# Optimization experiments

Hardware: AMD Instinct MI355X
Metric: run time of the kernel (lower is better)

## Reference

```python
import jax, jax.numpy as jnp
import numpy as np

D_MODEL = 1024
N_HEADS = 16
N_GROUPS = 4
D_K = D_MODEL // N_HEADS
HEADS_PER_GROUP = N_HEADS // N_GROUPS


def rope(x):
    # x: [b, s, d]; rotate using half-split concat (NOT interleaved), matching source
    s, d = x.shape[1], x.shape[2]
    theta = 1.0 / (10000.0 ** (jnp.arange(d // 2, dtype=jnp.float32) / (d // 2)))
    ang = jnp.arange(s, dtype=jnp.float32)[:, None] * theta[None, :]  # [s, d/2]
    cos, sin = jnp.cos(ang), jnp.sin(ang)
    xe, xo = x[..., 0::2], x[..., 1::2]
    return jnp.concatenate([xe * cos - xo * sin, xe * sin + xo * cos], axis=-1)


def setup_inputs() -> dict:
    key = jax.random.key(0)
    k1, k2, k3, k4, k5 = jax.random.split(key, 5)
    b, s = 1, 2048
    scale = 0.02
    X = jax.random.normal(k1, (b, s, D_MODEL), dtype=jnp.float32)
    W_q = jax.random.normal(k2, (D_MODEL, D_MODEL), dtype=jnp.float32) * scale
    W_k = jax.random.normal(k3, (N_GROUPS * D_K, D_MODEL), dtype=jnp.float32) * scale
    W_v = jax.random.normal(k4, (N_GROUPS * D_K, D_MODEL), dtype=jnp.float32) * scale
    W_o = jax.random.normal(k5, (D_MODEL, D_MODEL), dtype=jnp.float32) * scale
    return {"X": X, "W_q": W_q, "W_k": W_k, "W_v": W_v, "W_o": W_o}


def reference(X, W_q, W_k, W_v, W_o):
    b, s, _ = X.shape
    Xr = rope(X)
    Q = (Xr @ W_q.T).reshape(b, s, N_HEADS, D_K).transpose(0, 2, 1, 3)
    K = (Xr @ W_k.T).reshape(b, s, N_GROUPS, D_K).transpose(0, 2, 1, 3)
    V = (Xr @ W_v.T).reshape(b, s, N_GROUPS, D_K).transpose(0, 2, 1, 3)
    Q = Q.reshape(b, N_GROUPS, HEADS_PER_GROUP, s, D_K)
    scores = jnp.einsum('bghsd,bgtd->bghst', Q, K) / jnp.sqrt(jnp.float32(D_K))
    mask = jnp.triu(jnp.ones((s, s), dtype=scores.dtype), k=1) * (-1e9)
    attn = jax.nn.softmax(scores + mask, axis=-1)
    out = jnp.einsum('bghst,bgtd->bghsd', attn, V)  # [b,g,h,s,dk]
    out = out.reshape(b, N_HEADS, s, D_K).transpose(0, 2, 1, 3).reshape(b, s, D_MODEL)
    return out @ W_o.T
```

## Files before the change

kernel.cpp:

```cpp
#include <hip/hip_runtime.h>
#include <hip/hip_bf16.h>

#define S_LEN   2048
#define D_MODEL 1024
#define N_HEADS 16
#define N_GROUPS 4
#define D_K     64
#define KV_DIM  (N_GROUPS * D_K)

typedef __hip_bfloat16 bf16;
typedef unsigned short u16;
typedef __attribute__((ext_vector_type(8))) short bfrag;
typedef __attribute__((ext_vector_type(4))) float ffrag;
typedef __attribute__((ext_vector_type(4))) unsigned int u32x4;

__device__ __forceinline__ float b2f(u16 u) {
    return __uint_as_float(((unsigned)u) << 16);
}
__device__ __forceinline__ u16 f2bu(float f) {
    bf16 h = __float2bfloat16(f);
    return __builtin_bit_cast(u16, h);
}
__device__ __forceinline__ unsigned cvt_pk_bf16(float lo, float hi) {
    unsigned r;
    asm("v_cvt_pk_bf16_f32 %0, %1, %2" : "=v"(r) : "v"(lo), "v"(hi));
    return r;
}
__device__ __forceinline__ float max3f(float a, float b, float c) {
    float d;
    asm("v_max3_f32 %0, %1, %2, %3" : "=v"(d) : "v"(a), "v"(b), "v"(c));
    return d;
}
__device__ __forceinline__ float ex2(float x) {
#if __has_builtin(__builtin_amdgcn_exp2f)
    return __builtin_amdgcn_exp2f(x);
#else
    return __expf(x * 0.69314718f);
#endif
}

typedef __attribute__((address_space(3))) u16 lds_u16;
typedef __attribute__((address_space(1))) const u16 glb_u16;
__device__ __forceinline__ void gld_lds16(const u16* g, u16* l) {
    __builtin_amdgcn_global_load_lds((glb_u16*)g, (lds_u16*)l, 16, 0, 0);
}

__device__ __forceinline__ int probe_f32(const u16* p) {
    int lane = threadIdx.x & 63;
    int e0 = (p[lane] >> 7) & 0xFF;
    int e1 = (p[lane + 64] >> 7) & 0xFF;
    int c = ((e0 < 100 || e0 > 140) ? 1 : 0) + ((e1 < 100 || e1 > 140) ? 1 : 0);
    unsigned long long b1 = __ballot(c >= 1);
    unsigned long long b2 = __ballot(c >= 2);
    return ((__popcll(b1) + __popcll(b2)) > 16) ? 1 : 0;
}

__global__ void probe5_kernel(const u16* __restrict__ p0, const u16* __restrict__ p1,
                              const u16* __restrict__ p2, const u16* __restrict__ p3,
                              const u16* __restrict__ p4, int* __restrict__ mode) {
    if (blockIdx.x != 0) return;
    const u16* ps[5] = {p0, p1, p2, p3, p4};
    int lane = threadIdx.x & 63;
    for (int t = 0; t < 5; t++) {
        int e0 = (ps[t][lane] >> 7) & 0xFF;
        int e1 = (ps[t][lane + 64] >> 7) & 0xFF;
        int c = ((e0 < 100 || e0 > 140) ? 1 : 0) + ((e1 < 100 || e1 > 140) ? 1 : 0);
        unsigned long long b1 = __ballot(c >= 1);
        unsigned long long b2 = __ballot(c >= 2);
        if (lane == 0) mode[t] = ((__popcll(b1) + __popcll(b2)) > 16) ? 1 : 0;
    }
}

__global__ __launch_bounds__(512)
void prep_kernel(const void* __restrict__ Xin, u16* __restrict__ Xr,
                 const void* __restrict__ Wq, const void* __restrict__ Wk,
                 const void* __restrict__ Wv, const void* __restrict__ Wo,
                 u16* __restrict__ WB, u16* __restrict__ WoB) {
    int b = blockIdx.x;
    if (b < S_LEN) {
        int md = probe_f32((const u16*)Xin);
        int i = b;
        int j = threadIdx.x;
        float freq = ex2(-(float)j * 0.025952563241307518f);
        float ang  = (float)i * freq;
        float sv, cv;
        sincosf(ang, &sv, &cv);
        int base = i * D_MODEL;
        float xe, xo;
        if (md) {
            float2 xv = *(const float2*)&((const float*)Xin)[base + 2 * j];
            xe = xv.x; xo = xv.y;
        } else {
            ushort2 xv = *(const ushort2*)&((const u16*)Xin)[base + 2 * j];
            xe = b2f(xv.x); xo = b2f(xv.y);
        }
        Xr[base + j]       = f2bu(xe * cv - xo * sv);
        Xr[base + 512 + j] = f2bu(xe * sv + xo * cv);
    } else {
        int bid = b - S_LEN;
        const void* src; u16* dst; int goff;
        if (bid < 256)      { src = Wq; dst = WB;               goff = bid; }
        else if (bid < 320) { src = Wk; dst = WB + 1024 * 1024; goff = bid - 256; }
        else if (bid < 384) { src = Wv; dst = WB + 1280 * 1024; goff = bid - 320; }
        else                { src = Wo; dst = WoB;              goff = bid - 384; }
        int md = probe_f32((const u16*)src);
        size_t g = (size_t)goff * 512 + threadIdx.x;
        if (md) {
            const float* f = (const float*)src + g * 8;
            float4 v0 = *(const float4*)f;
            float4 v1 = *(const float4*)(f + 4);
            u16 t[8] = {f2bu(v0.x), f2bu(v0.y), f2bu(v0.z), f2bu(v0.w),
                        f2bu(v1.x), f2bu(v1.y), f2bu(v1.z), f2bu(v1.w)};
            *(uint4*)(dst + g * 8) = *(const uint4*)t;
        } else {
            *(uint4*)(dst + g * 8) = *(const uint4*)((const u16*)src + g * 8);
        }
    }
}

__global__ __launch_bounds__(512)
void rope_kernel(const void* __restrict__ Xin, u16* __restrict__ Xr) {
    int md = probe_f32((const u16*)Xin);
    int i = blockIdx.x;
    int j = threadIdx.x;
    float freq = ex2(-(float)j * 0.025952563241307518f);
    float ang  = (float)i * freq;
    float sv, cv;
    sincosf(ang, &sv, &cv);
    int base = i * D_MODEL;
    float xe, xo;
    if (md) {
        float2 xv = *(const float2*)&((const float*)Xin)[base + 2 * j];
        xe = xv.x; xo = xv.y;
    } else {
        ushort2 xv = *(const ushort2*)&((const u16*)Xin)[base + 2 * j];
        xe = b2f(xv.x); xo = b2f(xv.y);
    }
    Xr[base + j]       = f2bu(xe * cv - xo * sv);
    Xr[base + 512 + j] = f2bu(xe * sv + xo * cv);
}

template<int MODE>
__global__ __launch_bounds__(256)
void gemm_fast(const u16* __restrict__ A, const u16* __restrict__ WBm,
               u16* __restrict__ Qm, u16* __restrict__ Km, u16* __restrict__ Vm,
               float* __restrict__ Cf) {
    __shared__ u16 As[2][8192];
    __shared__ u16 Bs[2][4096];
    const int tid = threadIdx.x;
    const int w = tid >> 6, lane = tid & 63, quad = lane >> 4, lcol = lane & 15;

    const int flat = blockIdx.y * gridDim.x + blockIdx.x;
    const int cpx  = (gridDim.x * gridDim.y) >> 3;
    const int ns   = (flat & 7) * cpx + (flat >> 3);
    const int m0 = (ns / gridDim.x) * 128;
    const int n0 = (ns % gridDim.x) * 64;

    const int arl   = lane >> 3;
    const int colsw = ((lane & 7) ^ arl) * 8;

    const u16* ap[4]; const u16* bp[2];
    #pragma unroll
    for (int c = 0; c < 4; c++)
        ap[c] = A + (size_t)(m0 + (c * 4 + w) * 8 + arl) * 1024 + colsw;
    #pragma unroll
    for (int c = 0; c < 2; c++)
        bp[c] = WBm + (size_t)(n0 + (c * 4 + w) * 8 + arl) * 1024 + colsw;

    const int abase = (w * 32 + lcol) * 64;
    const int koff0 = (quad * 8) ^ ((lcol & 7) * 8);
    const int koff1 = koff0 ^ 32;

    ffrag acc[2][4];
    #pragma unroll
    for (int rf = 0; rf < 2; rf++)
        #pragma unroll
        for (int ct = 0; ct < 4; ct++) acc[rf][ct] = (ffrag)0.0f;

    #pragma unroll
    for (int c = 0; c < 4; c++) gld_lds16(ap[c], &As[0][(c * 4 + w) * 512]);
    #pragma unroll
    for (int c = 0; c < 2; c++) gld_lds16(bp[c], &Bs[0][(c * 4 + w) * 512]);
    __syncthreads();

    int cur = 0;
    for (int k0 = 0; k0 < D_MODEL; k0 += 64) {
        if (k0 + 64 < D_MODEL) {
            const int nb = cur ^ 1;
            #pragma unroll
            for (int c = 0; c < 4; c++)
                gld_lds16(ap[c] + k0 + 64, &As[nb][(c * 4 + w) * 512]);
            #pragma unroll
            for (int c = 0; c < 2; c++)
                gld_lds16(bp[c] + k0 + 64, &Bs[nb][(c * 4 + w) * 512]);
        }

        const u16* Ab = &As[cur][0];
        const u16* Bb = &Bs[cur][0];
        const bfrag a00 = *(const bfrag*)&Ab[abase + koff0];
        const bfrag a10 = *(const bfrag*)&Ab[abase + 1024 + koff0];
        const bfrag a01 = *(const bfrag*)&Ab[abase + koff1];
        const bfrag a11 = *(const bfrag*)&Ab[abase + 1024 + koff1];
        #pragma unroll
        for (int ct = 0; ct < 4; ct++) {
            const int bb = (ct * 16 + lcol) * 64;
            const bfrag b0 = *(const bfrag*)&Bb[bb + koff0];
            acc[0][ct] = __builtin_amdgcn_mfma_f32_16x16x32_bf16(a00, b0, acc[0][ct], 0, 0, 0);
            acc[1][ct] = __builtin_amdgcn_mfma_f32_16x16x32_bf16(a10, b0, acc[1][ct], 0, 0, 0);
            const bfrag b1 = *(const bfrag*)&Bb[bb + koff1];
            acc[0][ct] = __builtin_amdgcn_mfma_f32_16x16x32_bf16(a01, b1, acc[0][ct], 0, 0, 0);
            acc[1][ct] = __builtin_amdgcn_mfma_f32_16x16x32_bf16(a11, b1, acc[1][ct], 0, 0, 0);
        }
        __syncthreads();
        cur ^= 1;
    }

    if (MODE == 0) {
        if (n0 < 1280) {
            u16* Cp; int ldc, nc;
            if (n0 < 1024) { Cp = Qm; ldc = 1024; nc = n0; }
            else           { Cp = Km; ldc = 256;  nc = n0 - 1024; }
            #pragma unroll
            for (int rf = 0; rf < 2; rf++)
                #pragma unroll
                for (int ct = 0; ct < 4; ct++)
                    #pragma unroll
                    for (int r = 0; r < 4; r++) {
                        int row = m0 + w * 32 + rf * 16 + quad * 4 + r;
                        Cp[(size_t)row * ldc + nc + ct * 16 + lcol] = f2bu(acc[rf][ct][r]);
                    }
        } else {
            const int nc = n0 - 1280;
            #pragma unroll
            for (int rf = 0; rf < 2; rf++)
                #pragma unroll
                for (int ct = 0; ct < 4; ct++)
                    #pragma unroll
                    for (int r = 0; r < 4; r++) {
                        int row = m0 + w * 32 + rf * 16 + quad * 4 + r;
                        int col = nc + ct * 16 + lcol;
                        Vm[(size_t)col * S_LEN + row] = f2bu(acc[rf][ct][r]);
                    }
        }
    } else {
        #pragma unroll
        for (int rf = 0; rf < 2; rf++)
            #pragma unroll
            for (int ct = 0; ct < 4; ct++)
                #pragma unroll
                for (int r = 0; r < 4; r++) {
                    int row = m0 + w * 32 + rf * 16 + quad * 4 + r;
                    Cf[(size_t)row * D_MODEL + n0 + ct * 16 + lcol] = acc[rf][ct][r];
                }
    }
}

__device__ __forceinline__ void stageB(u16* dst, const void* Bv, size_t off, int md) {
    if (md) {
        const float* Bf = (const float*)Bv;
        float4 b0 = *(const float4*)&Bf[off];
        float4 b1 = *(const float4*)&Bf[off + 4];
        u16 t[8] = {f2bu(b0.x), f2bu(b0.y), f2bu(b0.z), f2bu(b0.w),
                    f2bu(b1.x), f2bu(b1.y), f2bu(b1.z), f2bu(b1.w)};
        *(uint4*)dst = *(const uint4*)t;
    } else {
        *(uint4*)dst = *(const uint4*)&((const u16*)Bv)[off];
    }
}

__global__ __launch_bounds__(256)
void qkv_mfma(const u16* __restrict__ Xr, const void* __restrict__ Wq,
              const void* __restrict__ Wk, const void* __restrict__ Wv,
              u16* __restrict__ Qm, u16* __restrict__ Km, u16* __restrict__ Vm,
              const int* __restrict__ mode) {
    __shared__ u16 As[128][36];
    __shared__ u16 Bs[64][36];
    const int tid = threadIdx.x;
    const int w = tid >> 6, lane = tid & 63, quad = lane >> 4, lcol = lane & 15;
    const int m0 = blockIdx.y * 128;
    const int n0 = blockIdx.x * 64;

    const void* Bv; int nb, md;
    if (n0 < 1024)       { Bv = Wq; nb = n0;        md = mode[1]; }
    else if (n0 < 1280)  { Bv = Wk; nb = n0 - 1024; md = mode[2]; }
    else                 { Bv = Wv; nb = n0 - 1280; md = mode[3]; }

    ffrag acc[2][4];
    #pragma unroll
    for (int rf = 0; rf < 2; rf++)
        #pragma unroll
        for (int ct = 0; ct < 4; ct++) acc[rf][ct] = (ffrag)0.0f;

    const int arow = tid >> 2, akc = tid & 3;
    for (int k0 = 0; k0 < D_MODEL; k0 += 32) {
        *(uint4*)&As[arow][akc * 8] =
            *(const uint4*)&Xr[(size_t)(m0 + arow) * D_MODEL + k0 + akc * 8];
        *(uint4*)&As[arow + 64][akc * 8] =
            *(const uint4*)&Xr[(size_t)(m0 + arow + 64) * D_MODEL + k0 + akc * 8];
        stageB(&Bs[arow][akc * 8], Bv, (size_t)(nb + arow) * D_MODEL + k0 + akc * 8, md);
        __syncthreads();
        const bfrag a0 = *(const bfrag*)&As[w * 32 + lcol][quad * 8];
        const bfrag a1 = *(const bfrag*)&As[w * 32 + 16 + lcol][quad * 8];
        #pragma unroll
        for (int ct = 0; ct < 4; ct++) {
            const bfrag b = *(const bfrag*)&Bs[ct * 16 + lcol][quad * 8];
            acc[0][ct] = __builtin_amdgcn_mfma_f32_16x16x32_bf16(a0, b, acc[0][ct], 0, 0, 0);
            acc[1][ct] = __builtin_amdgcn_mfma_f32_16x16x32_bf16(a1, b, acc[1][ct], 0, 0, 0);
        }
        __syncthreads();
    }

    if (n0 < 1280) {
        u16* Cp; int ldc, nc;
        if (n0 < 1024) { Cp = Qm; ldc = 1024; nc = n0; }
        else           { Cp = Km; ldc = 256;  nc = n0 - 1024; }
        #pragma unroll
        for (int rf = 0; rf < 2; rf++)
            #pragma unroll
            for (int ct = 0; ct < 4; ct++)
                #pragma unroll
                for (int r = 0; r < 4; r++) {
                    int row = m0 + w * 32 + rf * 16 + quad * 4 + r;
                    Cp[(size_t)row * ldc + nc + ct * 16 + lcol] = f2bu(acc[rf][ct][r]);
                }
    } else {
        const int nc = n0 - 1280;
        #pragma unroll
        for (int rf = 0; rf < 2; rf++)
            #pragma unroll
            for (int ct = 0; ct < 4; ct++)
                #pragma unroll
                for (int r = 0; r < 4; r++) {
                    int row = m0 + w * 32 + rf * 16 + quad * 4 + r;
                    int col = nc + ct * 16 + lcol;
                    Vm[(size_t)col * S_LEN + row] = f2bu(acc[rf][ct][r]);
                }
    }
}

__global__ __launch_bounds__(256)
void oproj_mfma(const u16* __restrict__ A, const void* __restrict__ B,
                float* __restrict__ C, const int* __restrict__ mode) {
    __shared__ u16 As[128][36];
    __shared__ u16 Bs[64][36];
    const int tid = threadIdx.x;
    const int w = tid >> 6, lane = tid & 63, quad = lane >> 4, lcol = lane & 15;
    const int m0 = blockIdx.y * 128;
    const int n0 = blockIdx.x * 64;
    const int md = mode[4];

    ffrag acc[2][4];
    #pragma unroll
    for (int rf = 0; rf < 2; rf++)
        #pragma unroll
        for (int ct = 0; ct < 4; ct++) acc[rf][ct] = (ffrag)0.0f;

    const int arow = tid >> 2, akc = tid & 3;
    for (int k0 = 0; k0 < D_MODEL; k0 += 32) {
        *(uint4*)&As[arow][akc * 8] =
            *(const uint4*)&A[(size_t)(m0 + arow) * D_MODEL + k0 + akc * 8];
        *(uint4*)&As[arow + 64][akc * 8] =
            *(const uint4*)&A[(size_t)(m0 + arow + 64) * D_MODEL + k0 + akc * 8];
        stageB(&Bs[arow][akc * 8], B, (size_t)(n0 + arow) * D_MODEL + k0 + akc * 8, md);
        __syncthreads();
        const bfrag a0 = *(const bfrag*)&As[w * 32 + lcol][quad * 8];
        const bfrag a1 = *(const bfrag*)&As[w * 32 + 16 + lcol][quad * 8];
        #pragma unroll
        for (int ct = 0; ct < 4; ct++) {
            const bfrag b = *(const bfrag*)&Bs[ct * 16 + lcol][quad * 8];
            acc[0][ct] = __builtin_amdgcn_mfma_f32_16x16x32_bf16(a0, b, acc[0][ct], 0, 0, 0);
            acc[1][ct] = __builtin_amdgcn_mfma_f32_16x16x32_bf16(a1, b, acc[1][ct], 0, 0, 0);
        }
        __syncthreads();
    }

    #pragma unroll
    for (int rf = 0; rf < 2; rf++)
        #pragma unroll
        for (int ct = 0; ct < 4; ct++)
            #pragma unroll
            for (int r = 0; r < 4; r++) {
                int row = m0 + w * 32 + rf * 16 + quad * 4 + r;
                C[(size_t)row * D_MODEL + n0 + ct * 16 + lcol] = acc[rf][ct][r];
            }
}

template<int CS, int SF>
__global__ __launch_bounds__(256)
void attn_part(const u16* __restrict__ Q, const u16* __restrict__ K,
               const u16* __restrict__ Vt, float* __restrict__ OpF,
               u16* __restrict__ OpH, float2* __restrict__ ml2) {
    const int bid = blockIdx.x;
    const int cidx = bid >> 4;
    const int h = bid & 15;
    const int g = h >> 2;

    int i, c;
    if (CS == 3) {
        if (cidx < 8)       { i = cidx;                  c = 0; }
        else if (cidx < 24) { i = 8 + ((cidx - 8) >> 1); c = (cidx - 8) & 1; }
        else if (cidx < 48) { int q = (cidx - 24) / 3;   i = 16 + q; c = (cidx - 24) - 3 * q; }
        else                { i = 24 + ((cidx - 48) >> 2); c = (cidx - 48) & 3; }
    } else {
        if (cidx < 16) { i = cidx; c = 0; }
        else           { i = 16 + ((cidx - 16) >> 1); c = (cidx - 16) & 1; }
    }
    const int i0 = i * 64;
    const int tile0 = c << CS;
    const int tlast = min(i, ((c + 1) << CS) - 1);
    const int nt = tlast - tile0 + 1;

    const int tid  = threadIdx.x;
    const int w    = tid >> 6;
    const int lane = tid & 63;
    const int quad = lane >> 4;
    const int lcol = lane & 15;

    __shared__ u16 Ks[2][64][72];
    __shared__ u16 Vts[2][64][72];

    const int qi = i0 + w * 16 + lcol;
    const bfrag qb0 = *(const bfrag*)&Q[(size_t)qi * D_MODEL + h * 64 + quad * 8];
    const bfrag qb1 = *(const bfrag*)&Q[(size_t)qi * D_MODEL + h * 64 + 32 + quad * 8];

    ffrag oacc[4];
    #pragma unroll
    for (int ct = 0; ct < 4; ct++) oacc[ct] = (ffrag)0.0f;
    float m_run = -1e30f, l_run = 0.0f;

    const int key0 = tid & 63, dc0 = tid >> 6;
    const int vd0 = tid >> 3, vch = tid & 7;
    const int vpos0 = 32 * (vch >> 2) + 16 * (vch & 1) + 4 * ((vch >> 1) & 1);
    const u16* vbase0 = &Vt[(size_t)(g * 64 + vd0) * S_LEN];
    const u16* vbase1 = &Vt[(size_t)(g * 64 + vd0 + 32) * S_LEN];

    int jp = tile0 * 64;
    uint4 kpre0 = *(const uint4*)&K[(size_t)(jp + key0) * KV_DIM + g * 64 + dc0 * 8];
    uint4 kpre1 = *(const uint4*)&K[(size_t)(jp + key0) * KV_DIM + g * 64 + (dc0 + 4) * 8];
    uint4 vpre0 = *(const uint4*)&vbase0[jp + vch * 8];
    uint4 vpre1 = *(const uint4*)&vbase1[jp + vch * 8];

    {
        *(uint4*)&Ks[0][key0][dc0 * 8]       = kpre0;
        *(uint4*)&Ks[0][key0][(dc0 + 4) * 8] = kpre1;
        *(uint2*)&Vts[0][vd0][vpos0]          = make_uint2(vpre0.x, vpre0.y);
        *(uint2*)&Vts[0][vd0][vpos0 + 8]      = make_uint2(vpre0.z, vpre0.w);
        *(uint2*)&Vts[0][vd0 + 32][vpos0]     = make_uint2(vpre1.x, vpre1.y);
        *(uint2*)&Vts[0][vd0 + 32][vpos0 + 8] = make_uint2(vpre1.z, vpre1.w);
    }

    const float CF = 0.18033688f;
    int cur = 0;

    for (int tt = 0; tt < nt; tt++) {
        const int j0 = (tile0 + tt) * 64;

        if (tt + 1 < nt) {
            const int j0n = (tile0 + tt + 1) * 64;
            kpre0 = *(const uint4*)&K[(size_t)(j0n + key0) * KV_DIM + g * 64 + dc0 * 8];
            kpre1 = *(const uint4*)&K[(size_t)(j0n + key0) * KV_DIM + g * 64 + (dc0 + 4) * 8];
            vpre0 = *(const uint4*)&vbase0[j0n + vch * 8];
            vpre1 = *(const uint4*)&vbase1[j0n + vch * 8];
        }
        __syncthreads();

        ffrag sacc[4];
        #pragma unroll
        for (int ct = 0; ct < 4; ct++) sacc[ct] = (ffrag)0.0f;
        __builtin_amdgcn_s_setprio(1);
        #pragma unroll
        for (int ct = 0; ct < 4; ct++) {
            const bfrag kb0 = *(const bfrag*)&Ks[cur][ct * 16 + lcol][quad * 8];
            sacc[ct] = __builtin_amdgcn_mfma_f32_16x16x32_bf16(kb0, qb0, sacc[ct], 0, 0, 0);
            const bfrag kb1 = *(const bfrag*)&Ks[cur][ct * 16 + lcol][32 + quad * 8];
            sacc[ct] = __builtin_amdgcn_mfma_f32_16x16x32_bf16(kb1, qb1, sacc[ct], 0, 0, 0);
        }
        __builtin_amdgcn_s_setprio(0);

        float sv[4][4];
        if (tile0 + tt == i) {
            #pragma unroll
            for (int ct = 0; ct < 4; ct++)
                #pragma unroll
                for (int r = 0; r < 4; r++) {
                    int kj = j0 + ct * 16 + quad * 4 + r;
                    sv[ct][r] = (kj <= qi) ? sacc[ct][r] : -1e30f;
                }
        } else {
            #pragma unroll
            for (int ct = 0; ct < 4; ct++)
                #pragma unroll
                for (int r = 0; r < 4; r++) sv[ct][r] = sacc[ct][r];
        }

        float t0 = max3f(sv[0][0], sv[0][1], sv[0][2]);
        float t1 = max3f(sv[0][3], sv[1][0], sv[1][1]);
        float t2 = max3f(sv[1][2], sv[1][3], sv[2][0]);
        float t3 = max3f(sv[2][1], sv[2][2], sv[2][3]);
        float t4 = max3f(sv[3][0], sv[3][1], sv[3][2]);
        float mx = fmaxf(max3f(t0, t1, t2), max3f(t3, t4, sv[3][3]));
        mx = fmaxf(mx, __shfl_xor(mx, 16, 64));
        mx = fmaxf(mx, __shfl_xor(mx, 32, 64));

        if (!__all(mx <= m_run + 44.0f)) {
            float mnew = fmaxf(m_run, mx);
            float al = ex2((m_run - mnew) * CF);
            m_run = mnew;
            l_run *= al;
            #pragma unroll
            for (int r = 0; r < 4; r++) {
                float ar = __shfl(al, quad * 4 + r, 64);
                #pragma unroll
                for (int ct = 0; ct < 4; ct++) oacc[ct][r] *= ar;
            }
        }

        const float mc = m_run * CF;
        float rs = 0.0f;
        #pragma unroll
        for (int ct = 0; ct < 4; ct++)
            #pragma unroll
            for (int r = 0; r < 4; r++) {
                float p = ex2(sv[ct][r] * CF - mc);
                sv[ct][r] = p;
                rs += p;
            }
        rs += __shfl_xor(rs, 16, 64);
        rs += __shfl_xor(rs, 32, 64);
        l_run += rs;

        u32x4 pw0, pw1;
        pw0[0] = cvt_pk_bf16(sv[0][0], sv[0][1]);
        pw0[1] = cvt_pk_bf16(sv[0][2], sv[0][3]);
        pw0[2] = cvt_pk_bf16(sv[1][0], sv[1][1]);
        pw0[3] = cvt_pk_bf16(sv[1][2], sv[1][3]);
        pw1[0] = cvt_pk_bf16(sv[2][0], sv[2][1]);
        pw1[1] = cvt_pk_bf16(sv[2][2], sv[2][3]);
        pw1[2] = cvt_pk_bf16(sv[3][0], sv[3][1]);
        pw1[3] = cvt_pk_bf16(sv[3][2], sv[3][3]);
        const bfrag pa0 = __builtin_bit_cast(bfrag, pw0);
        const bfrag pa1 = __builtin_bit_cast(bfrag, pw1);

        __builtin_amdgcn_s_setprio(1);
        #pragma unroll
        for (int ct = 0; ct < 4; ct++) {
            const bfrag vb0 = *(const bfrag*)&Vts[cur][ct * 16 + lcol][quad * 8];
            oacc[ct] = __builtin_amdgcn_mfma_f32_16x16x32_bf16(pa0, vb0, oacc[ct], 0, 0, 0);
            const bfrag vb1 = *(const bfrag*)&Vts[cur][ct * 16 + lcol][32 + quad * 8];
            oacc[ct] = __builtin_amdgcn_mfma_f32_16x16x32_bf16(pa1, vb1, oacc[ct], 0, 0, 0);
        }
        __builtin_amdgcn_s_setprio(0);

        if (tt + 1 < nt) {
            const int nb = cur ^ 1;
            *(uint4*)&Ks[nb][key0][dc0 * 8]       = kpre0;
            *(uint4*)&Ks[nb][key0][(dc0 + 4) * 8] = kpre1;
            *(uint2*)&Vts[nb][vd0][vpos0]          = make_uint2(vpre0.x, vpre0.y);
            *(uint2*)&Vts[nb][vd0][vpos0 + 8]      = make_uint2(vpre0.z, vpre0.w);
            *(uint2*)&Vts[nb][vd0 + 32][vpos0]     = make_uint2(vpre1.x, vpre1.y);
            *(uint2*)&Vts[nb][vd0 + 32][vpos0 + 8] = make_uint2(vpre1.z, vpre1.w);
        }
        cur ^= 1;
    }

    #pragma unroll
    for (int ct = 0; ct < 4; ct++)
        #pragma unroll
        for (int r = 0; r < 4; r++) {
            int row = w * 16 + quad * 4 + r;
            size_t off = (size_t)bid * 4096 + row * 64 + ct * 16 + lcol;
            if (SF) OpF[off] = oacc[ct][r];
            else    OpH[off] = f2bu(oacc[ct][r]);
        }
    if (quad == 0)
        ml2[(size_t)bid * 64 + w * 16 + lcol] = make_float2(m_run * 0.125f, l_run);
}

template<int CS, int SF>
__global__ __launch_bounds__(256)
void attn_combine(const float* __restrict__ OpF, const u16* __restrict__ OpH,
                  const float2* __restrict__ ml2, u16* __restrict__ Om) {
    const int row = blockIdx.x;
    const int i = row >> 6;
    const int r = row & 63;
    const int t = threadIdx.x;
    const int h = t >> 4;
    const int d = (t & 15) * 4;
    const int nc = (i >> CS) + 1;
    int pfx;
    if (CS == 3)
        pfx = (i < 8) ? i : (i < 16) ? 8 + 2 * (i - 8)
            : (i < 24) ? 24 + 3 * (i - 16) : 48 + 4 * (i - 24);
    else
        pfx = (i < 16) ? i : 16 + 2 * (i - 16);

    float M = -1e30f;
    for (int c = 0; c < nc; c++) {
        float2 m = ml2[(size_t)((pfx + c) * 16 + h) * 64 + r];
        M = fmaxf(M, m.x);
    }
    float L = 0.0f;
    float acc[4] = {0.0f, 0.0f, 0.0f, 0.0f};
    for (int c = 0; c < nc; c++) {
        float2 m = ml2[(size_t)((pfx + c) * 16 + h) * 64 + r];
        float wgt = __expf(m.x - M);
        L += m.y * wgt;
        size_t off = (size_t)((pfx + c) * 16 + h) * 4096 + r * 64 + d;
        if (SF) {
            float4 v = *(const float4*)&OpF[off];
            acc[0] += v.x * wgt; acc[1] += v.y * wgt;
            acc[2] += v.z * wgt; acc[3] += v.w * wgt;
        } else {
            ushort4 v = *(const ushort4*)&OpH[off];
            acc[0] += b2f(v.x) * wgt; acc[1] += b2f(v.y) * wgt;
            acc[2] += b2f(v.z) * wgt; acc[3] += b2f(v.w) * wgt;
        }
    }
    float inv = 1.0f / L;
    #pragma unroll
    for (int k = 0; k < 4; k++)
        Om[(size_t)row * D_MODEL + h * 64 + d + k] = f2bu(acc[k] * inv);
}

extern "C" void kernel_launch(void* const* d_in, const int* in_sizes, int n_in,
                              void* d_out, int out_size, void* d_ws, size_t ws_size,
                              hipStream_t stream) {
    const void* X  = d_in[0];
    const void* Wq = d_in[1];
    const void* Wk = d_in[2];
    const void* Wv = d_in[3];
    const void* Wo = d_in[4];
    float* out = (float*)d_out;

    u16* XrB = (u16*)d_out;

    int* mode = (int*)d_ws;
    u16* Qm = (u16*)((char*)d_ws + 64);
    u16* Km = Qm + (size_t)S_LEN * D_MODEL;
    u16* Vm = Km + (size_t)S_LEN * KV_DIM;
    u16* Om = Vm + (size_t)S_LEN * KV_DIM;

    const size_t needA    = 10485824ULL + 20971520ULL + 655360ULL;
    const size_t needFull = needA + 3145728ULL + 2097152ULL;

    if (ws_size >= needFull) {
        float*  OpF = (float*)((char*)d_ws + 10485824);
        float2* ml2 = (float2*)((char*)d_ws + 10485824 + 20971520);
        u16*    WB  = (u16*)((char*)d_ws + needA);
        u16*    WoB = WB + (size_t)1536 * 1024;

        prep_kernel<<<S_LEN + 640, 512, 0, stream>>>(X, XrB, Wq, Wk, Wv, Wo, WB, WoB);
        gemm_fast<0><<<dim3(24, 16), 256, 0, stream>>>(XrB, WB, Qm, Km, Vm, nullptr);
        attn_part<3, 1><<<80 * 16, 256, 0, stream>>>(Qm, Km, Vm, OpF, nullptr, ml2);
        attn_combine<3, 1><<<S_LEN, 256, 0, stream>>>(OpF, nullptr, ml2, Om);
        gemm_fast<1><<<dim3(16, 16), 256, 0, stream>>>(Om, WoB, nullptr, nullptr, nullptr, out);
    } else {
        rope_kernel<<<S_LEN, 512, 0, stream>>>(X, XrB);
        probe5_kernel<<<1, 64, 0, stream>>>(
            (const u16*)X, (const u16*)Wq, (const u16*)Wk, (const u16*)Wv,
            (const u16*)Wo, mode);
        qkv_mfma<<<dim3((D_MODEL + 2 * KV_DIM) / 64, S_LEN / 128), 256, 0, stream>>>(
            XrB, Wq, Wk, Wv, Qm, Km, Vm, mode);
        if (ws_size >= needA) {
            float*  OpF = (float*)((char*)d_ws + 10485824);
            float2* ml2 = (float2*)((char*)d_ws + 10485824 + 20971520);
            attn_part<3, 1><<<80 * 16, 256, 0, stream>>>(Qm, Km, Vm, OpF, nullptr, ml2);
            attn_combine<3, 1><<<S_LEN, 256, 0, stream>>>(OpF, nullptr, ml2, Om);
        } else {
            u16*    OpH = (u16*)d_out;
            float2* ml2 = (float2*)((char*)d_out + (size_t)768 * 4096 * 2);
            attn_part<4, 0><<<48 * 16, 256, 0, stream>>>(Qm, Km, Vm, nullptr, OpH, ml2);
            attn_combine<4, 0><<<S_LEN, 256, 0, stream>>>(nullptr, OpH, ml2, Om);
        }
        oproj_mfma<<<dim3(D_MODEL / 64, S_LEN / 128), 256, 0, stream>>>(Om, Wo, out, mode);
    }
}
```

Baseline: 141.2 us.

## Schedule full attention chunks longest-first and defer softmax rescale past PV MFMA

Reorders the split-KV attention block mapping so full 8-tile chunks are launched before the partial diagonal chunks, ordered from largest work down. The combine kernel gets a matching position function. This is meant to reduce tail imbalance across CUs. It also starts the running max at zero and moves the online-softmax rescale after the P·V MFMAs, so the rescale branch no longer sits on the critical path before the exponentials. The trade-off is that probabilities are briefly computed against a stale max and may reach large magnitudes before they are rescaled.

```diff
diff --git a/kernel.cpp b/kernel.cpp
--- a/kernel.cpp
+++ b/kernel.cpp
@@ -43,6 +43,13 @@
 typedef __attribute__((address_space(1))) const u16 glb_u16;
 __device__ __forceinline__ void gld_lds16(const u16* g, u16* l) {
     __builtin_amdgcn_global_load_lds((glb_u16*)g, (lds_u16*)l, 16, 0, 0);
+}
+
+__device__ __forceinline__ int pos3(int i, int c) {
+    int d = i - 8 * c;
+    if (d >= 7)
+        return (c == 0) ? i - 7 : (c == 1) ? 10 + i : (c == 2) ? 19 + i : 51;
+    return 52 + (6 - d) * 4 + c;
 }
 
 __device__ __forceinline__ int probe_f32(const u16* p) {
@@ -397,10 +404,11 @@
 
     int i, c;
     if (CS == 3) {
-        if (cidx < 8)       { i = cidx;                  c = 0; }
-        else if (cidx < 24) { i = 8 + ((cidx - 8) >> 1); c = (cidx - 8) & 1; }
-        else if (cidx < 48) { int q = (cidx - 24) / 3;   i = 16 + q; c = (cidx - 24) - 3 * q; }
-        else                { i = 24 + ((cidx - 48) >> 2); c = (cidx - 48) & 3; }
+        if (cidx < 25)       { c = 0; i = cidx + 7; }
+        else if (cidx < 42)  { c = 1; i = cidx - 10; }
+        else if (cidx < 51)  { c = 2; i = cidx - 19; }
+        else if (cidx == 51) { c = 3; i = 31; }
+        else { int t = cidx - 52; int dd = 6 - (t >> 2); c = t & 3; i = 8 * c + dd; }
     } else {
         if (cidx < 16) { i = cidx; c = 0; }
         else           { i = 16 + ((cidx - 16) >> 1); c = (cidx - 16) & 1; }
@@ -426,7 +434,7 @@
     ffrag oacc[4];
     #pragma unroll
     for (int ct = 0; ct < 4; ct++) oacc[ct] = (ffrag)0.0f;
-    float m_run = -1e30f, l_run = 0.0f;
+    float m_run = 0.0f, l_run = 0.0f;
 
     const int key0 = tid & 63, dc0 = tid >> 6;
     const int vd0 = tid >> 3, vch = tid & 7;
@@ -501,19 +509,6 @@
         float mx = fmaxf(max3f(t0, t1, t2), max3f(t3, t4, sv[3][3]));
         mx = fmaxf(mx, __shfl_xor(mx, 16, 64));
         mx = fmaxf(mx, __shfl_xor(mx, 32, 64));
-
-        if (!__all(mx <= m_run + 44.0f)) {
-            float mnew = fmaxf(m_run, mx);
-            float al = ex2((m_run - mnew) * CF);
-            m_run = mnew;
-            l_run *= al;
-            #pragma unroll
-            for (int r = 0; r < 4; r++) {
-                float ar = __shfl(al, quad * 4 + r, 64);
-                #pragma unroll
-                for (int ct = 0; ct < 4; ct++) oacc[ct][r] *= ar;
-            }
-        }
 
         const float mc = m_run * CF;
         float rs = 0.0f;
@@ -551,6 +546,19 @@
         }
         __builtin_amdgcn_s_setprio(0);
 
+        if (!__all(mx <= m_run + 44.0f)) {
+            float mnew = fmaxf(m_run, mx);
+            float al = ex2((m_run - mnew) * CF);
+            l_run *= al;
+            #pragma unroll
+            for (int r = 0; r < 4; r++) {
+                float ar = __shfl(al, quad * 4 + r, 64);
+                #pragma unroll
+                for (int ct = 0; ct < 4; ct++) oacc[ct][r] *= ar;
+            }
+            m_run = mnew;
+        }
+
         if (tt + 1 < nt) {
             const int nb = cur ^ 1;
             *(uint4*)&Ks[nb][key0][dc0 * 8]       = kpre0;
@@ -587,25 +595,21 @@
     const int h = t >> 4;
     const int d = (t & 15) * 4;
     const int nc = (i >> CS) + 1;
-    int pfx;
-    if (CS == 3)
-        pfx = (i < 8) ? i : (i < 16) ? 8 + 2 * (i - 8)
-            : (i < 24) ? 24 + 3 * (i - 16) : 48 + 4 * (i - 24);
-    else
-        pfx = (i < 16) ? i : 16 + 2 * (i - 16);
 
     float M = -1e30f;
     for (int c = 0; c < nc; c++) {
-        float2 m = ml2[(size_t)((pfx + c) * 16 + h) * 64 + r];
+        int pos = (CS == 3) ? pos3(i, c) : ((i < 16) ? i : 16 + 2 * (i - 16)) + c;
+        float2 m = ml2[(size_t)(pos * 16 + h) * 64 + r];
         M = fmaxf(M, m.x);
     }
     float L = 0.0f;
     float acc[4] = {0.0f, 0.0f, 0.0f, 0.0f};
     for (int c = 0; c < nc; c++) {
-        float2 m = ml2[(size_t)((pfx + c) * 16 + h) * 64 + r];
+        int pos = (CS == 3) ? pos3(i, c) : ((i < 16) ? i : 16 + 2 * (i - 16)) + c;
+        float2 m = ml2[(size_t)(pos * 16 + h) * 64 + r];
         float wgt = __expf(m.x - M);
         L += m.y * wgt;
-        size_t off = (size_t)((pfx + c) * 16 + h) * 4096 + r * 64 + d;
+        size_t off = (size_t)(pos * 16 + h) * 4096 + r * 64 + d;
         if (SF) {
             float4 v = *(const float4*)&OpF[off];
             acc[0] += v.x * wgt; acc[1] += v.y * wgt;
```

Measured after the change: 138.7 us. No clear change (-1.8%).

## Process 128 query rows per attention block to reuse K/V tiles

Applied to the files above, without the earlier changes.

Each attention work item now covers two 64-row query tiles (A and B) that share every K/V tile loaded into LDS, which halves the number of K/V loads and blocks. The causal chunk scheduling and the combine kernel's indexing are remapped for 128-row items, with a reordered work list so that longer chunks are issued first. Softmax rescaling is deferred until after the PV MFMA, starting from a running max of zero. Launch bounds request 4 waves per SIMD. Register pressure roughly doubles and there are half as many blocks, which may reduce occupancy and parallelism.

```diff
diff --git a/kernel.cpp b/kernel.cpp
--- a/kernel.cpp
+++ b/kernel.cpp
@@ -43,6 +43,13 @@
 typedef __attribute__((address_space(1))) const u16 glb_u16;
 __device__ __forceinline__ void gld_lds16(const u16* g, u16* l) {
     __builtin_amdgcn_global_load_lds((glb_u16*)g, (lds_u16*)l, 16, 0, 0);
+}
+
+__device__ __forceinline__ int posCS3(int i, int c) {
+    if (i >= 4 * c + 3)
+        return (c == 0) ? i - 3 : (c == 1) ? i + 6 : (c == 2) ? i + 11 : 27;
+    int dd = i - 4 * c + 1;
+    return 28 + (3 - dd) * 4 + c;
 }
 
 __device__ __forceinline__ int probe_f32(const u16* p) {
@@ -386,7 +393,7 @@
 }
 
 template<int CS, int SF>
-__global__ __launch_bounds__(256)
+__global__ __launch_bounds__(256, 4)
 void attn_part(const u16* __restrict__ Q, const u16* __restrict__ K,
                const u16* __restrict__ Vt, float* __restrict__ OpF,
                u16* __restrict__ OpH, float2* __restrict__ ml2) {
@@ -397,17 +404,18 @@
 
     int i, c;
     if (CS == 3) {
-        if (cidx < 8)       { i = cidx;                  c = 0; }
-        else if (cidx < 24) { i = 8 + ((cidx - 8) >> 1); c = (cidx - 8) & 1; }
-        else if (cidx < 48) { int q = (cidx - 24) / 3;   i = 16 + q; c = (cidx - 24) - 3 * q; }
-        else                { i = 24 + ((cidx - 48) >> 2); c = (cidx - 48) & 3; }
+        if (cidx < 13)       { c = 0; i = cidx + 3; }
+        else if (cidx < 22)  { c = 1; i = cidx - 6; }
+        else if (cidx < 27)  { c = 2; i = cidx - 11; }
+        else if (cidx == 27) { c = 3; i = 15; }
+        else { int t = cidx - 28; int dd = 3 - (t >> 2); c = t & 3; i = 4 * c + dd - 1; }
     } else {
-        if (cidx < 16) { i = cidx; c = 0; }
-        else           { i = 16 + ((cidx - 16) >> 1); c = (cidx - 16) & 1; }
-    }
-    const int i0 = i * 64;
+        if (cidx < 8) { i = cidx; c = 0; }
+        else          { i = 8 + ((cidx - 8) >> 1); c = (cidx - 8) & 1; }
+    }
+    const int i0 = i * 128;
     const int tile0 = c << CS;
-    const int tlast = min(i, ((c + 1) << CS) - 1);
+    const int tlast = min(2 * i + 1, ((c + 1) << CS) - 1);
     const int nt = tlast - tile0 + 1;
 
     const int tid  = threadIdx.x;
@@ -419,14 +427,18 @@
     __shared__ u16 Ks[2][64][72];
     __shared__ u16 Vts[2][64][72];
 
-    const int qi = i0 + w * 16 + lcol;
-    const bfrag qb0 = *(const bfrag*)&Q[(size_t)qi * D_MODEL + h * 64 + quad * 8];
-    const bfrag qb1 = *(const bfrag*)&Q[(size_t)qi * D_MODEL + h * 64 + 32 + quad * 8];
-
-    ffrag oacc[4];
-    #pragma unroll
-    for (int ct = 0; ct < 4; ct++) oacc[ct] = (ffrag)0.0f;
-    float m_run = -1e30f, l_run = 0.0f;
+    const int qiA = i0 + w * 16 + lcol;
+    const int qiB = qiA + 64;
+    const bfrag qbA0 = *(const bfrag*)&Q[(size_t)qiA * D_MODEL + h * 64 + quad * 8];
+    const bfrag qbA1 = *(const bfrag*)&Q[(size_t)qiA * D_MODEL + h * 64 + 32 + quad * 8];
+    const bfrag qbB0 = *(const bfrag*)&Q[(size_t)qiB * D_MODEL + h * 64 + quad * 8];
+    const bfrag qbB1 = *(const bfrag*)&Q[(size_t)qiB * D_MODEL + h * 64 + 32 + quad * 8];
+
+    ffrag oaccA[4], oaccB[4];
+    #pragma unroll
+    for (int ct = 0; ct < 4; ct++) { oaccA[ct] = (ffrag)0.0f; oaccB[ct] = (ffrag)0.0f; }
+    float m_runA = 0.0f, l_runA = 0.0f;
+    float m_runB = 0.0f, l_runB = 0.0f;
 
     const int key0 = tid & 63, dc0 = tid >> 6;
     const int vd0 = tid >> 3, vch = tid & 7;
@@ -453,10 +465,11 @@
     int cur = 0;
 
     for (int tt = 0; tt < nt; tt++) {
-        const int j0 = (tile0 + tt) * 64;
+        const int tj = tile0 + tt;
+        const int j0 = tj * 64;
 
         if (tt + 1 < nt) {
-            const int j0n = (tile0 + tt + 1) * 64;
+            const int j0n = (tj + 1) * 64;
             kpre0 = *(const uint4*)&K[(size_t)(j0n + key0) * KV_DIM + g * 64 + dc0 * 8];
             kpre1 = *(const uint4*)&K[(size_t)(j0n + key0) * KV_DIM + g * 64 + (dc0 + 4) * 8];
             vpre0 = *(const uint4*)&vbase0[j0n + vch * 8];
@@ -464,92 +477,157 @@
         }
         __syncthreads();
 
-        ffrag sacc[4];
-        #pragma unroll
-        for (int ct = 0; ct < 4; ct++) sacc[ct] = (ffrag)0.0f;
+        ffrag saccA[4], saccB[4];
+        #pragma unroll
+        for (int ct = 0; ct < 4; ct++) { saccA[ct] = (ffrag)0.0f; saccB[ct] = (ffrag)0.0f; }
         __builtin_amdgcn_s_setprio(1);
         #pragma unroll
         for (int ct = 0; ct < 4; ct++) {
             const bfrag kb0 = *(const bfrag*)&Ks[cur][ct * 16 + lcol][quad * 8];
-            sacc[ct] = __builtin_amdgcn_mfma_f32_16x16x32_bf16(kb0, qb0, sacc[ct], 0, 0, 0);
+            saccA[ct] = __builtin_amdgcn_mfma_f32_16x16x32_bf16(kb0, qbA0, saccA[ct], 0, 0, 0);
+            saccB[ct] = __builtin_amdgcn_mfma_f32_16x16x32_bf16(kb0, qbB0, saccB[ct], 0, 0, 0);
             const bfrag kb1 = *(const bfrag*)&Ks[cur][ct * 16 + lcol][32 + quad * 8];
-            sacc[ct] = __builtin_amdgcn_mfma_f32_16x16x32_bf16(kb1, qb1, sacc[ct], 0, 0, 0);
+            saccA[ct] = __builtin_amdgcn_mfma_f32_16x16x32_bf16(kb1, qbA1, saccA[ct], 0, 0, 0);
+            saccB[ct] = __builtin_amdgcn_mfma_f32_16x16x32_bf16(kb1, qbB1, saccB[ct], 0, 0, 0);
         }
         __builtin_amdgcn_s_setprio(0);
 
-        float sv[4][4];
-        if (tile0 + tt == i) {
+        float svA[4][4];
+        if (tj >= 2 * i) {
             #pragma unroll
             for (int ct = 0; ct < 4; ct++)
                 #pragma unroll
                 for (int r = 0; r < 4; r++) {
                     int kj = j0 + ct * 16 + quad * 4 + r;
-                    sv[ct][r] = (kj <= qi) ? sacc[ct][r] : -1e30f;
+                    svA[ct][r] = (kj <= qiA) ? saccA[ct][r] : -1e30f;
                 }
         } else {
             #pragma unroll
             for (int ct = 0; ct < 4; ct++)
                 #pragma unroll
-                for (int r = 0; r < 4; r++) sv[ct][r] = sacc[ct][r];
-        }
-
-        float t0 = max3f(sv[0][0], sv[0][1], sv[0][2]);
-        float t1 = max3f(sv[0][3], sv[1][0], sv[1][1]);
-        float t2 = max3f(sv[1][2], sv[1][3], sv[2][0]);
-        float t3 = max3f(sv[2][1], sv[2][2], sv[2][3]);
-        float t4 = max3f(sv[3][0], sv[3][1], sv[3][2]);
-        float mx = fmaxf(max3f(t0, t1, t2), max3f(t3, t4, sv[3][3]));
-        mx = fmaxf(mx, __shfl_xor(mx, 16, 64));
-        mx = fmaxf(mx, __shfl_xor(mx, 32, 64));
-
-        if (!__all(mx <= m_run + 44.0f)) {
-            float mnew = fmaxf(m_run, mx);
-            float al = ex2((m_run - mnew) * CF);
-            m_run = mnew;
-            l_run *= al;
+                for (int r = 0; r < 4; r++) svA[ct][r] = saccA[ct][r];
+        }
+        float tA0 = max3f(svA[0][0], svA[0][1], svA[0][2]);
+        float tA1 = max3f(svA[0][3], svA[1][0], svA[1][1]);
+        float tA2 = max3f(svA[1][2], svA[1][3], svA[2][0]);
+        float tA3 = max3f(svA[2][1], svA[2][2], svA[2][3]);
+        float tA4 = max3f(svA[3][0], svA[3][1], svA[3][2]);
+        float mxA = fmaxf(max3f(tA0, tA1, tA2), max3f(tA3, tA4, svA[3][3]));
+        mxA = fmaxf(mxA, __shfl_xor(mxA, 16, 64));
+        mxA = fmaxf(mxA, __shfl_xor(mxA, 32, 64));
+
+        const float mcA = m_runA * CF;
+        float rsA = 0.0f;
+        #pragma unroll
+        for (int ct = 0; ct < 4; ct++)
+            #pragma unroll
+            for (int r = 0; r < 4; r++) {
+                float p = ex2(svA[ct][r] * CF - mcA);
+                svA[ct][r] = p;
+                rsA += p;
+            }
+        rsA += __shfl_xor(rsA, 16, 64);
+        rsA += __shfl_xor(rsA, 32, 64);
+        l_runA += rsA;
+
+        u32x4 pwA0, pwA1;
+        pwA0[0] = cvt_pk_bf16(svA[0][0], svA[0][1]);
+        pwA0[1] = cvt_pk_bf16(svA[0][2], svA[0][3]);
+        pwA0[2] = cvt_pk_bf16(svA[1][0], svA[1][1]);
+        pwA0[3] = cvt_pk_bf16(svA[1][2], svA[1][3]);
+        pwA1[0] = cvt_pk_bf16(svA[2][0], svA[2][1]);
+        pwA1[1] = cvt_pk_bf16(svA[2][2], svA[2][3]);
+        pwA1[2] = cvt_pk_bf16(svA[3][0], svA[3][1]);
+        pwA1[3] = cvt_pk_bf16(svA[3][2], svA[3][3]);
+        const bfrag paA0 = __builtin_bit_cast(bfrag, pwA0);
+        const bfrag paA1 = __builtin_bit_cast(bfrag, pwA1);
+
+        float svB[4][4];
+        if (tj == 2 * i + 1) {
+            #pragma unroll
+            for (int ct = 0; ct < 4; ct++)
+                #pragma unroll
+                for (int r = 0; r < 4; r++) {
+                    int kj = j0 + ct * 16 + quad * 4 + r;
+                    svB[ct][r] = (kj <= qiB) ? saccB[ct][r] : -1e30f;
+                }
+        } else {
+            #pragma unroll
+            for (int ct = 0; ct < 4; ct++)
+                #pragma unroll
+                for (int r = 0; r < 4; r++) svB[ct][r] = saccB[ct][r];
+        }
+        float tB0 = max3f(svB[0][0], svB[0][1], svB[0][2]);
+        float tB1 = max3f(svB[0][3], svB[1][0], svB[1][1]);
+        float tB2 = max3f(svB[1][2], svB[1][3], svB[2][0]);
+        float tB3 = max3f(svB[2][1], svB[2][2], svB[2][3]);
+        float tB4 = max3f(svB[3][0], svB[3][1], svB[3][2]);
+        float mxB = fmaxf(max3f(tB0, tB1, tB2), max3f(tB3, tB4, svB[3][3]));
+        mxB = fmaxf(mxB, __shfl_xor(mxB, 16, 64));
+        mxB = fmaxf(mxB, __shfl_xor(mxB, 32, 64));
+
+        const float mcB = m_runB * CF;
+        float rsB = 0.0f;
+        #pragma unroll
+        for (int ct = 0; ct < 4; ct++)
+            #pragma unroll
+            for (int r = 0; r < 4; r++) {
+                float p = ex2(svB[ct][r] * CF - mcB);
+                svB[ct][r] = p;
+                rsB += p;
+            }
+        rsB += __shfl_xor(rsB, 16, 64);
+        rsB += __shfl_xor(rsB, 32, 64);
+        l_runB += rsB;
+
+        u32x4 pwB0, pwB1;
+        pwB0[0] = cvt_pk_bf16(svB[0][0], svB[0][1]);
+        pwB0[1] = cvt_pk_bf16(svB[0][2], svB[0][3]);
+        pwB0[2] = cvt_pk_bf16(svB[1][0], svB[1][1]);
+        pwB0[3] = cvt_pk_bf16(svB[1][2], svB[1][3]);
+        pwB1[0] = cvt_pk_bf16(svB[2][0], svB[2][1]);
+        pwB1[1] = cvt_pk_bf16(svB[2][2], svB[2][3]);
+        pwB1[2] = cvt_pk_bf16(svB[3][0], svB[3][1]);
+        pwB1[3] = cvt_pk_bf16(svB[3][2], svB[3][3]);
+        const bfrag paB0 = __builtin_bit_cast(bfrag, pwB0);
+        const bfrag paB1 = __builtin_bit_cast(bfrag, pwB1);
+
+        __builtin_amdgcn_s_setprio(1);
+        #pragma unroll
+        for (int ct = 0; ct < 4; ct++) {
+            const bfrag vb0 = *(const bfrag*)&Vts[cur][ct * 16 + lcol][quad * 8];
+            oaccA[ct] = __builtin_amdgcn_mfma_f32_16x16x32_bf16(paA0, vb0, oaccA[ct], 0, 0, 0);
+            oaccB[ct] = __builtin_amdgcn_mfma_f32_16x16x32_bf16(paB0, vb0, oaccB[ct], 0, 0, 0);
+            const bfrag vb1 = *(const bfrag*)&Vts[cur][ct * 16 + lcol][32 + quad * 8];
+            oaccA[ct] = __builtin_amdgcn_mfma_f32_16x16x32_bf16(paA1, vb1, oaccA[ct], 0, 0, 0);
+            oaccB[ct] = __builtin_amdgcn_mfma_f32_16x16x32_bf16(paB1, vb1, oaccB[ct], 0, 0, 0);
+        }
+        __builtin_amdgcn_s_setprio(0);
+
+        if (!__all(mxA <= m_runA + 44.0f)) {
+            float mnew = fmaxf(m_runA, mxA);
+            float al = ex2((m_runA - mnew) * CF);
+            l_runA *= al;
             #pragma unroll
             for (int r = 0; r < 4; r++) {
                 float ar = __shfl(al, quad * 4 + r, 64);
                 #pragma unroll
-                for (int ct = 0; ct < 4; ct++) oacc[ct][r] *= ar;
+                for (int ct = 0; ct < 4; ct++) oaccA[ct][r] *= ar;
             }
-        }
-
-        const float mc = m_run * CF;
-        float rs = 0.0f;
-        #pragma unroll
-        for (int ct = 0; ct < 4; ct++)
+            m_runA = mnew;
+        }
+        if (!__all(mxB <= m_runB + 44.0f)) {
+            float mnew = fmaxf(m_runB, mxB);
+            float al = ex2((m_runB - mnew) * CF);
+            l_runB *= al;
             #pragma unroll
             for (int r = 0; r < 4; r++) {
-                float p = ex2(sv[ct][r] * CF - mc);
-                sv[ct][r] = p;
-                rs += p;
+                float ar = __shfl(al, quad * 4 + r, 64);
+                #pragma unroll
+                for (int ct = 0; ct < 4; ct++) oaccB[ct][r] *= ar;
             }
-        rs += __shfl_xor(rs, 16, 64);
-        rs += __shfl_xor(rs, 32, 64);
-        l_run += rs;
-
-        u32x4 pw0, pw1;
-        pw0[0] = cvt_pk_bf16(sv[0][0], sv[0][1]);
-        pw0[1] = cvt_pk_bf16(sv[0][2], sv[0][3]);
-        pw0[2] = cvt_pk_bf16(sv[1][0], sv[1][1]);
-        pw0[3] = cvt_pk_bf16(sv[1][2], sv[1][3]);
-        pw1[0] = cvt_pk_bf16(sv[2][0], sv[2][1]);
-        pw1[1] = cvt_pk_bf16(sv[2][2], sv[2][3]);
-        pw1[2] = cvt_pk_bf16(sv[3][0], sv[3][1]);
-        pw1[3] = cvt_pk_bf16(sv[3][2], sv[3][3]);
-        const bfrag pa0 = __builtin_bit_cast(bfrag, pw0);
-        const bfrag pa1 = __builtin_bit_cast(bfrag, pw1);
-
-        __builtin_amdgcn_s_setprio(1);
-        #pragma unroll
-        for (int ct = 0; ct < 4; ct++) {
-            const bfrag vb0 = *(const bfrag*)&Vts[cur][ct * 16 + lcol][quad * 8];
-            oacc[ct] = __builtin_amdgcn_mfma_f32_16x16x32_bf16(pa0, vb0, oacc[ct], 0, 0, 0);
-            const bfrag vb1 = *(const bfrag*)&Vts[cur][ct * 16 + lcol][32 + quad * 8];
-            oacc[ct] = __builtin_amdgcn_mfma_f32_16x16x32_bf16(pa1, vb1, oacc[ct], 0, 0, 0);
-        }
-        __builtin_amdgcn_s_setprio(0);
+            m_runB = mnew;
+        }
 
         if (tt + 1 < nt) {
             const int nb = cur ^ 1;
@@ -567,13 +645,16 @@
     for (int ct = 0; ct < 4; ct++)
         #pragma unroll
         for (int r = 0; r < 4; r++) {
-            int row = w * 16 + quad * 4 + r;
-            size_t off = (size_t)bid * 4096 + row * 64 + ct * 16 + lcol;
-            if (SF) OpF[off] = oacc[ct][r];
-            else    OpH[off] = f2bu(oacc[ct][r]);
-        }
-    if (quad == 0)
-        ml2[(size_t)bid * 64 + w * 16 + lcol] = make_float2(m_run * 0.125f, l_run);
+            int rowA = w * 16 + quad * 4 + r;
+            size_t offA = (size_t)bid * 8192 + rowA * 64 + ct * 16 + lcol;
+            size_t offB = offA + 4096;
+            if (SF) { OpF[offA] = oaccA[ct][r]; OpF[offB] = oaccB[ct][r]; }
+            else    { OpH[offA] = f2bu(oaccA[ct][r]); OpH[offB] = f2bu(oaccB[ct][r]); }
+        }
+    if (quad == 0) {
+        ml2[(size_t)bid * 128 + w * 16 + lcol]      = make_float2(m_runA * 0.125f, l_runA);
+        ml2[(size_t)bid * 128 + 64 + w * 16 + lcol] = make_float2(m_runB * 0.125f, l_runB);
+    }
 }
 
 template<int CS, int SF>
@@ -581,31 +662,27 @@
 void attn_combine(const float* __restrict__ OpF, const u16* __restrict__ OpH,
                   const float2* __restrict__ ml2, u16* __restrict__ Om) {
     const int row = blockIdx.x;
-    const int i = row >> 6;
-    const int r = row & 63;
+    const int i = row >> 7;
+    const int r = row & 127;
     const int t = threadIdx.x;
     const int h = t >> 4;
     const int d = (t & 15) * 4;
-    const int nc = (i >> CS) + 1;
-    int pfx;
-    if (CS == 3)
-        pfx = (i < 8) ? i : (i < 16) ? 8 + 2 * (i - 8)
-            : (i < 24) ? 24 + 3 * (i - 16) : 48 + 4 * (i - 24);
-    else
-        pfx = (i < 16) ? i : 16 + 2 * (i - 16);
+    const int nc = (CS == 3) ? ((2 * i + 1) >> 3) + 1 : ((2 * i + 1) >> 4) + 1;
 
     float M = -1e30f;
     for (int c = 0; c < nc; c++) {
-        float2 m = ml2[(size_t)((pfx + c) * 16 + h) * 64 + r];
+        int pos = (CS == 3) ? posCS3(i, c) : ((i < 8) ? i : 8 + 2 * (i - 8) + c);
+        float2 m = ml2[(size_t)(pos * 16 + h) * 128 + r];
         M = fmaxf(M, m.x);
     }
     float L = 0.0f;
     float acc[4] = {0.0f, 0.0f, 0.0f, 0.0f};
     for (int c = 0; c < nc; c++) {
-        float2 m = ml2[(size_t)((pfx + c) * 16 + h) * 64 + r];
+        int pos = (CS == 3) ? posCS3(i, c) : ((i < 8) ? i : 8 + 2 * (i - 8) + c);
+        float2 m = ml2[(size_t)(pos * 16 + h) * 128 + r];
         float wgt = __expf(m.x - M);
         L += m.y * wgt;
-        size_t off = (size_t)((pfx + c) * 16 + h) * 4096 + r * 64 + d;
+        size_t off = (size_t)(pos * 16 + h) * 8192 + r * 64 + d;
         if (SF) {
             float4 v = *(const float4*)&OpF[off];
             acc[0] += v.x * wgt; acc[1] += v.y * wgt;
@@ -651,7 +728,7 @@
 
         prep_kernel<<<S_LEN + 640, 512, 0, stream>>>(X, XrB, Wq, Wk, Wv, Wo, WB, WoB);
         gemm_fast<0><<<dim3(24, 16), 256, 0, stream>>>(XrB, WB, Qm, Km, Vm, nullptr);
-        attn_part<3, 1><<<80 * 16, 256, 0, stream>>>(Qm, Km, Vm, OpF, nullptr, ml2);
+        attn_part<3, 1><<<40 * 16, 256, 0, stream>>>(Qm, Km, Vm, OpF, nullptr, ml2);
         attn_combine<3, 1><<<S_LEN, 256, 0, stream>>>(OpF, nullptr, ml2, Om);
         gemm_fast<1><<<dim3(16, 16), 256, 0, stream>>>(Om, WoB, nullptr, nullptr, nullptr, out);
     } else {
@@ -664,12 +741,12 @@
         if (ws_size >= needA) {
             float*  OpF = (float*)((char*)d_ws + 10485824);
             float2* ml2 = (float2*)((char*)d_ws + 10485824 + 20971520);
-            attn_part<3, 1><<<80 * 16, 256, 0, stream>>>(Qm, Km, Vm, OpF, nullptr, ml2);
+            attn_part<3, 1><<<40 * 16, 256, 0, stream>>>(Qm, Km, Vm, OpF, nullptr, ml2);
             attn_combine<3, 1><<<S_LEN, 256, 0, stream>>>(OpF, nullptr, ml2, Om);
         } else {
             u16*    OpH = (u16*)d_out;
             float2* ml2 = (float2*)((char*)d_out + (size_t)768 * 4096 * 2);
-            attn_part<4, 0><<<48 * 16, 256, 0, stream>>>(Qm, Km, Vm, nullptr, OpH, ml2);
+            attn_part<4, 0><<<24 * 16, 256, 0, stream>>>(Qm, Km, Vm, nullptr, OpH, ml2);
             attn_combine<4, 0><<<S_LEN, 256, 0, stream>>>(nullptr, OpH, ml2, Om);
         }
         oproj_mfma<<<dim3(D_MODEL / 64, S_LEN / 128), 256, 0, stream>>>(Om, Wo, out, mode);
```

After: 136.4 us. -3.4%, faster.
